# Kernel tuning notes

Hardware: AMD Instinct MI355X
Metric: run time of the kernel (lower is better)

The kernel has to match this reference:

```python
import jax, jax.numpy as jnp
import numpy as np

B, S, HID = 4, 2048, 768
NUM_HEADS = 12
HEAD_DIM = HID // NUM_HEADS


def setup_inputs() -> dict:
    key = jax.random.key(0)
    ks = jax.random.split(key, 9)
    sc = 1.0 / np.sqrt(HID)
    return {
        "x":  jax.random.normal(ks[0], (B, S, HID), dtype=jnp.float32),
        "Wq": jax.random.normal(ks[1], (HID, HID), dtype=jnp.float32) * sc,
        "bq": jnp.zeros((HID,), dtype=jnp.float32),
        "Wk": jax.random.normal(ks[2], (HID, HID), dtype=jnp.float32) * sc,
        "bk": jnp.zeros((HID,), dtype=jnp.float32),
        "Wv": jax.random.normal(ks[3], (HID, HID), dtype=jnp.float32) * sc,
        "bv": jnp.zeros((HID,), dtype=jnp.float32),
        "Wo": jax.random.normal(ks[4], (HID, HID), dtype=jnp.float32) * sc,
        "bo": jnp.zeros((HID,), dtype=jnp.float32),
    }


def _split_heads(t):
    # [B, S, HID] -> [B, H, S, D]
    b, s, _ = t.shape
    return t.reshape(b, s, NUM_HEADS, HEAD_DIM).transpose(0, 2, 1, 3)


def reference(x, Wq, bq, Wk, bk, Wv, bv, Wo, bo):
    # QKV projections (torch Linear: y = x @ W.T + b; here W stored as [in, out])
    q = _split_heads(x @ Wq + bq)
    k = _split_heads(x @ Wk + bk)
    v = _split_heads(x @ Wv + bv)
    # scaled dot-product attention scores [B, H, S, S]
    scores = jnp.einsum("bhqd,bhkd->bhqk", q, k) / jnp.sqrt(jnp.float32(HEAD_DIM))
    attn = jax.nn.softmax(scores, axis=-1)
    # dropout prob is 0.0 in the source -> identity
    ctx = jnp.einsum("bhqk,bhkd->bhqd", attn, v)
    ctx = ctx.transpose(0, 2, 1, 3).reshape(x.shape[0], x.shape[1], HID)
    out = ctx @ Wo + bo
    return out, attn
```

## Files before the change

### kernel.cpp

```cpp
#include <hip/hip_runtime.h>
#include <hip/hip_bf16.h>

typedef __bf16 bf16;
typedef __bf16 bf16x8 __attribute__((ext_vector_type(8)));
typedef float  f32x4  __attribute__((ext_vector_type(4)));

#define NB   4
#define NS   2048
#define NH   12
#define ND   64
#define NHID 768
#define NM   (NB*NS)

__device__ __forceinline__ void async_cp16(void* lds, const void* g) {
  __builtin_amdgcn_global_load_lds(
      (const __attribute__((address_space(1))) void*)g,
      (__attribute__((address_space(3))) void*)lds, 16, 0, 0);
}

__device__ __forceinline__ f32x4 mfma16(bf16x8 a, bf16x8 b, f32x4 c) {
  return __builtin_amdgcn_mfma_f32_16x16x32_bf16(a, b, c, 0, 0, 0);
}

__global__ void k_cvt_x(const float4* __restrict__ x, bf16* __restrict__ o) {
  int i = blockIdx.x * 256 + threadIdx.x;
  float4 v = x[i];
  bf16* p = o + (size_t)i * 4;
  p[0] = (bf16)v.x; p[1] = (bf16)v.y; p[2] = (bf16)v.z; p[3] = (bf16)v.w;
}

__global__ void k_trans_w(const float* __restrict__ W0, const float* __restrict__ W1,
                          const float* __restrict__ W2, const float* __restrict__ W3,
                          bf16* __restrict__ T0, bf16* __restrict__ T1,
                          bf16* __restrict__ T2, bf16* __restrict__ T3) {
  int z = blockIdx.z;
  const float* W = (z==0)?W0:(z==1)?W1:(z==2)?W2:W3;
  bf16*        T = (z==0)?T0:(z==1)?T1:(z==2)?T2:T3;
  __shared__ float t[32][33];
  int tx = threadIdx.x & 31, ty = threadIdx.x >> 5;
  int n0 = blockIdx.x * 32, k0 = blockIdx.y * 32;
  for (int i = 0; i < 32; i += 8)
    t[ty + i][tx] = W[(size_t)(k0 + ty + i) * NHID + n0 + tx];
  __syncthreads();
  for (int i = 0; i < 32; i += 8)
    T[(size_t)(n0 + ty + i) * NHID + k0 + tx] = (bf16)t[tx][ty + i];
}

__launch_bounds__(256, 2)
__global__ void k_proj(const bf16* __restrict__ xb,
                       const bf16* __restrict__ Wtq, const bf16* __restrict__ Wtk,
                       const bf16* __restrict__ Wtv,
                       const float* __restrict__ bq, const float* __restrict__ bk,
                       const float* __restrict__ bv,
                       bf16* __restrict__ qo, bf16* __restrict__ ko, bf16* __restrict__ vto) {
  const int z = blockIdx.z;
  const bf16*  Wt   = (z==0)?Wtq:(z==1)?Wtk:Wtv;
  const float* bias = (z==0)?bq :(z==1)?bk :bv;
  __shared__ __align__(16) bf16 As[128*32];
  __shared__ __align__(16) bf16 Bs[128*32];
  const int tid = threadIdx.x, w = tid >> 6, l = tid & 63;
  const int m0 = blockIdx.y * 128, n0 = blockIdx.x * 128;

  const int lr = tid >> 2, lc = tid & 3;
  const bf16* agp[2]; const bf16* bgp[2]; char* alds[2]; char* blds[2];
  for (int i = 0; i < 2; i++) {
    int r = i * 64 + lr;
    int cl = lc ^ (r & 3);
    agp[i] = xb + (size_t)(m0 + r) * NHID + cl * 8;
    bgp[i] = Wt + (size_t)(n0 + r) * NHID + cl * 8;
    alds[i] = (char*)As + i * 4096 + w * 1024;
    blds[i] = (char*)Bs + i * 4096 + w * 1024;
  }
  const int fch = ((l >> 4) ^ (l & 3)) * 8;
  const int wm = (w >> 1) * 64, wn = (w & 1) * 64;
  int aoff[4], boff[4];
  for (int i = 0; i < 4; i++) {
    aoff[i] = (wm + i * 16 + (l & 15)) * 32 + fch;
    boff[i] = (wn + i * 16 + (l & 15)) * 32 + fch;
  }
  f32x4 acc[4][4];
  f32x4 zf = {0.f, 0.f, 0.f, 0.f};
  for (int i = 0; i < 4; i++) for (int j = 0; j < 4; j++) acc[i][j] = zf;

  for (int kt = 0; kt < NHID / 32; kt++) {
    __syncthreads();
    const size_t ko2 = (size_t)kt * 32;
    for (int i = 0; i < 2; i++) {
      async_cp16(alds[i], agp[i] + ko2);
      async_cp16(blds[i], bgp[i] + ko2);
    }
    __syncthreads();
    bf16x8 af[4], bfr[4];
    for (int i = 0; i < 4; i++) af[i]  = *(const bf16x8*)(As + aoff[i]);
    for (int i = 0; i < 4; i++) bfr[i] = *(const bf16x8*)(Bs + boff[i]);
    for (int i = 0; i < 4; i++)
      for (int j = 0; j < 4; j++)
        acc[i][j] = mfma16(af[i], bfr[j], acc[i][j]);
  }
  bf16* outp = (z==0)?qo:(z==1)?ko:vto;
  for (int i = 0; i < 4; i++) {
    int mrow0 = m0 + wm + i * 16 + (l >> 4) * 4;
    for (int j = 0; j < 4; j++) {
      int col = n0 + wn + j * 16 + (l & 15);
      float bb = bias[col];
      int h = col >> 6, d = col & 63;
      for (int r = 0; r < 4; r++) {
        int m = mrow0 + r;
        int b = m >> 11, s = m & 2047;
        float v = acc[i][j][r] + bb;
        size_t idx;
        if (z < 2) idx = ((size_t)(b * NH + h) * NS + s) * ND + d;
        else       idx = ((size_t)(b * NH + h) * ND + d) * NS + s;
        outp[idx] = (bf16)v;
      }
    }
  }
}

__launch_bounds__(256, 2)
__global__ void k_rowsum(const bf16* __restrict__ qg, const bf16* __restrict__ kg,
                         float* __restrict__ rowsum) {
  const int bh = blockIdx.y;
  const int q0 = blockIdx.x * 128;
  __shared__ __align__(16) bf16 Qs[128*64];
  __shared__ __align__(16) bf16 Ks[128*64];
  const int tid = threadIdx.x, w = tid >> 6, l = tid & 63;
  const int lr8 = tid >> 3, lc8 = tid & 7;

  const bf16* qbase = qg + ((size_t)bh * NS + q0) * ND;
  for (int i = 0; i < 4; i++) {
    int r = i * 32 + lr8;
    int cl = lc8 ^ (r & 7);
    async_cp16((char*)Qs + i * 4096 + w * 1024, qbase + (size_t)r * ND + cl * 8);
  }
  int aoff[2][2], boff[8][2];
  for (int rb = 0; rb < 2; rb++)
    for (int ks = 0; ks < 2; ks++) {
      int row = w * 32 + rb * 16 + (l & 15);
      int ph = (ks * 4 + (l >> 4)) ^ (l & 7);
      aoff[rb][ks] = row * 64 + ph * 8;
    }
  for (int cb = 0; cb < 8; cb++)
    for (int ks = 0; ks < 2; ks++) {
      int row = cb * 16 + (l & 15);
      int ph = (ks * 4 + (l >> 4)) ^ (l & 7);
      boff[cb][ks] = row * 64 + ph * 8;
    }
  bf16x8 aq[2][2];
  float rs[2][4];
  for (int rb = 0; rb < 2; rb++) for (int r = 0; r < 4; r++) rs[rb][r] = 0.f;

  for (int kt = 0; kt < NS / 128; kt++) {
    __syncthreads();
    const bf16* kbase = kg + ((size_t)bh * NS + kt * 128) * ND;
    for (int i = 0; i < 4; i++) {
      int r = i * 32 + lr8;
      int cl = lc8 ^ (r & 7);
      async_cp16((char*)Ks + i * 4096 + w * 1024, kbase + (size_t)r * ND + cl * 8);
    }
    __syncthreads();
    if (kt == 0)
      for (int rb = 0; rb < 2; rb++)
        for (int ks = 0; ks < 2; ks++)
          aq[rb][ks] = *(const bf16x8*)(Qs + aoff[rb][ks]);
    for (int cb = 0; cb < 8; cb++) {
      bf16x8 b0 = *(const bf16x8*)(Ks + boff[cb][0]);
      bf16x8 b1 = *(const bf16x8*)(Ks + boff[cb][1]);
      for (int rb = 0; rb < 2; rb++) {
        f32x4 acc = {0.f, 0.f, 0.f, 0.f};
        acc = mfma16(aq[rb][0], b0, acc);
        acc = mfma16(aq[rb][1], b1, acc);
        for (int r = 0; r < 4; r++) rs[rb][r] += __expf(acc[r] * 0.125f);
      }
    }
  }
  for (int m = 1; m < 16; m <<= 1)
    for (int rb = 0; rb < 2; rb++)
      for (int r = 0; r < 4; r++)
        rs[rb][r] += __shfl_xor(rs[rb][r], m, 64);
  if ((l & 15) == 0)
    for (int rb = 0; rb < 2; rb++)
      for (int r = 0; r < 4; r++)
        rowsum[(size_t)bh * NS + q0 + w * 32 + rb * 16 + (l >> 4) * 4 + r] = rs[rb][r];
}

__launch_bounds__(256, 2)
__global__ void k_attn(const bf16* __restrict__ qg, const bf16* __restrict__ kg,
                       const bf16* __restrict__ vtg, const float* __restrict__ rowsum,
                       float* __restrict__ attn, bf16* __restrict__ ctxo) {
  const int bh = blockIdx.y;
  const int q0 = blockIdx.x * 128;
  __shared__ __align__(16) bf16 Qs[128*64];
  __shared__ __align__(16) bf16 Ks[128*64];
  __shared__ __align__(16) bf16 Vs[64*128];
  __shared__ __align__(16) bf16 Ps[4][32*40];
  __shared__ float Rs[128];
  const int tid = threadIdx.x, w = tid >> 6, l = tid & 63;

  if (tid < 128) Rs[tid] = 1.f / rowsum[(size_t)bh * NS + q0 + tid];

  const int lr8 = tid >> 3, lc8 = tid & 7;
  const int lr16 = tid >> 4, lc16 = tid & 15;
  const bf16* qbase = qg + ((size_t)bh * NS + q0) * ND;
  for (int i = 0; i < 4; i++) {
    int r = i * 32 + lr8;
    int cl = lc8 ^ (r & 7);
    async_cp16((char*)Qs + i * 4096 + w * 1024, qbase + (size_t)r * ND + cl * 8);
  }
  int aoff[2][2], boff[8][2];
  for (int rb = 0; rb < 2; rb++)
    for (int ks = 0; ks < 2; ks++) {
      int row = w * 32 + rb * 16 + (l & 15);
      int ph = (ks * 4 + (l >> 4)) ^ (l & 7);
      aoff[rb][ks] = row * 64 + ph * 8;
    }
  for (int cb = 0; cb < 8; cb++)
    for (int ks = 0; ks < 2; ks++) {
      int row = cb * 16 + (l & 15);
      int ph = (ks * 4 + (l >> 4)) ^ (l & 7);
      boff[cb][ks] = row * 64 + ph * 8;
    }
  bf16x8 aq[2][2];
  float rv[2][4];
  f32x4 ctx[2][4];
  f32x4 zf = {0.f, 0.f, 0.f, 0.f};
  for (int i = 0; i < 2; i++) for (int j = 0; j < 4; j++) ctx[i][j] = zf;

  for (int kt = 0; kt < NS / 128; kt++) {
    __syncthreads();
    const bf16* kbase = kg + ((size_t)bh * NS + kt * 128) * ND;
    for (int i = 0; i < 4; i++) {
      int r = i * 32 + lr8;
      int cl = lc8 ^ (r & 7);
      async_cp16((char*)Ks + i * 4096 + w * 1024, kbase + (size_t)r * ND + cl * 8);
    }
    const bf16* vbase = vtg + (size_t)bh * ND * NS + (size_t)kt * 128;
    for (int i = 0; i < 4; i++) {
      int r = i * 16 + lr16;
      int cl = lc16 ^ (r & 15);
      async_cp16((char*)Vs + i * 4096 + w * 1024, vbase + (size_t)r * NS + cl * 8);
    }
    __syncthreads();
    if (kt == 0) {
      for (int rb = 0; rb < 2; rb++)
        for (int ks = 0; ks < 2; ks++)
          aq[rb][ks] = *(const bf16x8*)(Qs + aoff[rb][ks]);
      for (int rb = 0; rb < 2; rb++)
        for (int r = 0; r < 4; r++)
          rv[rb][r] = Rs[w * 32 + rb * 16 + (l >> 4) * 4 + r];
    }
    const size_t arow0 = (size_t)bh * NS + q0 + w * 32;
    for (int ks2 = 0; ks2 < 4; ks2++) {
      for (int cc = 0; cc < 2; cc++) {
        int cb = ks2 * 2 + cc;
        bf16x8 b0 = *(const bf16x8*)(Ks + boff[cb][0]);
        bf16x8 b1 = *(const bf16x8*)(Ks + boff[cb][1]);
        for (int rb = 0; rb < 2; rb++) {
          f32x4 acc = {0.f, 0.f, 0.f, 0.f};
          acc = mfma16(aq[rb][0], b0, acc);
          acc = mfma16(aq[rb][1], b1, acc);
          int rloc = rb * 16 + (l >> 4) * 4;
          for (int r = 0; r < 4; r++) {
            float p = __expf(acc[r] * 0.125f) * rv[rb][r];
            attn[(arow0 + rloc + r) * NS + (size_t)kt * 128 + cb * 16 + (l & 15)] = p;
            Ps[w][(rloc + r) * 40 + cc * 16 + (l & 15)] = (bf16)p;
          }
        }
      }
      bf16x8 pa[2];
      for (int rb = 0; rb < 2; rb++)
        pa[rb] = *(const bf16x8*)(&Ps[w][(rb * 16 + (l & 15)) * 40 + (l >> 4) * 8]);
      for (int db = 0; db < 4; db++) {
        int dd = db * 16 + (l & 15);
        int ph = (ks2 * 4 + (l >> 4)) ^ (l & 15);
        bf16x8 vb = *(const bf16x8*)(Vs + dd * 128 + ph * 8);
        for (int rb = 0; rb < 2; rb++)
          ctx[rb][db] = mfma16(pa[rb], vb, ctx[rb][db]);
      }
    }
  }
  const int b = bh / NH, h = bh - b * NH;
  for (int rb = 0; rb < 2; rb++) {
    int qrow0 = q0 + w * 32 + rb * 16 + (l >> 4) * 4;
    for (int db = 0; db < 4; db++) {
      int dd = db * 16 + (l & 15);
      for (int r = 0; r < 4; r++)
        ctxo[((size_t)(b * NS + qrow0 + r)) * NHID + h * ND + dd] = (bf16)ctx[rb][db][r];
    }
  }
}

__launch_bounds__(256, 2)
__global__ void k_oproj(const bf16* __restrict__ cb_, const bf16* __restrict__ Wto,
                        const float* __restrict__ bo, float* __restrict__ out) {
  __shared__ __align__(16) bf16 As[128*32];
  __shared__ __align__(16) bf16 Bs[128*32];
  const int tid = threadIdx.x, w = tid >> 6, l = tid & 63;
  const int m0 = blockIdx.y * 128, n0 = blockIdx.x * 128;
  const int lr = tid >> 2, lc = tid & 3;
  const bf16* agp[2]; const bf16* bgp[2]; char* alds[2]; char* blds[2];
  for (int i = 0; i < 2; i++) {
    int r = i * 64 + lr;
    int cl = lc ^ (r & 3);
    agp[i] = cb_ + (size_t)(m0 + r) * NHID + cl * 8;
    bgp[i] = Wto + (size_t)(n0 + r) * NHID + cl * 8;
    alds[i] = (char*)As + i * 4096 + w * 1024;
    blds[i] = (char*)Bs + i * 4096 + w * 1024;
  }
  const int fch = ((l >> 4) ^ (l & 3)) * 8;
  const int wm = (w >> 1) * 64, wn = (w & 1) * 64;
  int aoff[4], boff[4];
  for (int i = 0; i < 4; i++) {
    aoff[i] = (wm + i * 16 + (l & 15)) * 32 + fch;
    boff[i] = (wn + i * 16 + (l & 15)) * 32 + fch;
  }
  f32x4 acc[4][4];
  f32x4 zf = {0.f, 0.f, 0.f, 0.f};
  for (int i = 0; i < 4; i++) for (int j = 0; j < 4; j++) acc[i][j] = zf;

  for (int kt = 0; kt < NHID / 32; kt++) {
    __syncthreads();
    const size_t ko2 = (size_t)kt * 32;
    for (int i = 0; i < 2; i++) {
      async_cp16(alds[i], agp[i] + ko2);
      async_cp16(blds[i], bgp[i] + ko2);
    }
    __syncthreads();
    bf16x8 af[4], bfr[4];
    for (int i = 0; i < 4; i++) af[i]  = *(const bf16x8*)(As + aoff[i]);
    for (int i = 0; i < 4; i++) bfr[i] = *(const bf16x8*)(Bs + boff[i]);
    for (int i = 0; i < 4; i++)
      for (int j = 0; j < 4; j++)
        acc[i][j] = mfma16(af[i], bfr[j], acc[i][j]);
  }
  for (int i = 0; i < 4; i++) {
    int mrow0 = m0 + wm + i * 16 + (l >> 4) * 4;
    for (int j = 0; j < 4; j++) {
      int col = n0 + wn + j * 16 + (l & 15);
      float bb = bo[col];
      for (int r = 0; r < 4; r++)
        out[(size_t)(mrow0 + r) * NHID + col] = acc[i][j][r] + bb;
    }
  }
}

extern "C" void kernel_launch(void* const* d_in, const int* in_sizes, int n_in,
                              void* d_out, int out_size, void* d_ws, size_t ws_size,
                              hipStream_t stream) {
  const float* x  = (const float*)d_in[0];
  const float* Wq = (const float*)d_in[1];
  const float* bq = (const float*)d_in[2];
  const float* Wk = (const float*)d_in[3];
  const float* bk = (const float*)d_in[4];
  const float* Wv = (const float*)d_in[5];
  const float* bv = (const float*)d_in[6];
  const float* Wo = (const float*)d_in[7];
  const float* bo = (const float*)d_in[8];
  float* out  = (float*)d_out;
  float* attn = out + (size_t)NB * NS * NHID;

  char* ws = (char*)d_ws;
  const size_t XB = (size_t)NM * NHID * 2;
  const size_t WB = (size_t)NHID * NHID * 2;
  const size_t QB = (size_t)NB * NH * NS * ND * 2;
  bf16* xb  = (bf16*)(ws);
  bf16* Wtq = (bf16*)(ws + XB);
  bf16* Wtk = (bf16*)(ws + XB + WB);
  bf16* Wtv = (bf16*)(ws + XB + 2 * WB);
  bf16* Wto = (bf16*)(ws + XB + 3 * WB);
  bf16* qw  = (bf16*)(ws + XB + 4 * WB);
  bf16* kw  = (bf16*)(ws + XB + 4 * WB + QB);
  bf16* vtw = (bf16*)(ws + XB + 4 * WB + 2 * QB);
  bf16* ctx = (bf16*)(ws + XB + 4 * WB + 3 * QB);
  float* rsum = (float*)(ws + XB + 4 * WB + 4 * QB);

  hipLaunchKernelGGL(k_cvt_x, dim3(NM * NHID / 1024), dim3(256), 0, stream,
                     (const float4*)x, xb);
  hipLaunchKernelGGL(k_trans_w, dim3(24, 24, 4), dim3(256), 0, stream,
                     Wq, Wk, Wv, Wo, Wtq, Wtk, Wtv, Wto);
  hipLaunchKernelGGL(k_proj, dim3(NHID / 128, NM / 128, 3), dim3(256), 0, stream,
                     xb, Wtq, Wtk, Wtv, bq, bk, bv, qw, kw, vtw);
  hipLaunchKernelGGL(k_rowsum, dim3(NS / 128, NB * NH), dim3(256), 0, stream,
                     qw, kw, rsum);
  hipLaunchKernelGGL(k_attn, dim3(NS / 128, NB * NH), dim3(256), 0, stream,
                     qw, kw, vtw, rsum, attn, ctx);
  hipLaunchKernelGGL(k_oproj, dim3(NHID / 128, NM / 128), dim3(256), 0, stream,
                     ctx, Wto, bo, out);
}
```

Before: 1.088 ms.

## Double-buffer LDS tiles, remap block IDs for XCD locality, prioritise MFMA waves

```diff
diff --git a/kernel.cpp b/kernel.cpp
--- a/kernel.cpp
+++ b/kernel.cpp
@@ -20,6 +20,11 @@
 
 __device__ __forceinline__ f32x4 mfma16(bf16x8 a, bf16x8 b, f32x4 c) {
   return __builtin_amdgcn_mfma_f32_16x16x32_bf16(a, b, c, 0, 0, 0);
+}
+
+__device__ __forceinline__ void vm0_bar() {
+  asm volatile("s_waitcnt vmcnt(0)" ::: "memory");
+  __builtin_amdgcn_s_barrier();
 }
 
 __global__ void k_cvt_x(const float4* __restrict__ x, bf16* __restrict__ o) {
@@ -53,24 +58,33 @@
                        const float* __restrict__ bq, const float* __restrict__ bk,
                        const float* __restrict__ bv,
                        bf16* __restrict__ qo, bf16* __restrict__ ko, bf16* __restrict__ vto) {
-  const int z = blockIdx.z;
+  const int id = blockIdx.x;
+  const int kx = id & 7, sl = id >> 3;
+  const int my = (sl / 18) * 8 + kx;
+  const int r2 = sl % 18;
+  const int nx = r2 % 6, z = r2 / 6;
   const bf16*  Wt   = (z==0)?Wtq:(z==1)?Wtk:Wtv;
   const float* bias = (z==0)?bq :(z==1)?bk :bv;
-  __shared__ __align__(16) bf16 As[128*32];
-  __shared__ __align__(16) bf16 Bs[128*32];
+  __shared__ __align__(16) bf16 As[2][128*32];
+  __shared__ __align__(16) bf16 Bs[2][128*32];
   const int tid = threadIdx.x, w = tid >> 6, l = tid & 63;
-  const int m0 = blockIdx.y * 128, n0 = blockIdx.x * 128;
+  const int m0 = my * 128, n0 = nx * 128;
 
   const int lr = tid >> 2, lc = tid & 3;
-  const bf16* agp[2]; const bf16* bgp[2]; char* alds[2]; char* blds[2];
+  const bf16* agp[2]; const bf16* bgp[2];
   for (int i = 0; i < 2; i++) {
     int r = i * 64 + lr;
     int cl = lc ^ (r & 3);
     agp[i] = xb + (size_t)(m0 + r) * NHID + cl * 8;
     bgp[i] = Wt + (size_t)(n0 + r) * NHID + cl * 8;
-    alds[i] = (char*)As + i * 4096 + w * 1024;
-    blds[i] = (char*)Bs + i * 4096 + w * 1024;
-  }
+  }
+  auto stage = [&](int b, int kt) {
+    const size_t ko2 = (size_t)kt * 32;
+    for (int i = 0; i < 2; i++) {
+      async_cp16((char*)As + b * 8192 + i * 4096 + w * 1024, agp[i] + ko2);
+      async_cp16((char*)Bs + b * 8192 + i * 4096 + w * 1024, bgp[i] + ko2);
+    }
+  };
   const int fch = ((l >> 4) ^ (l & 3)) * 8;
   const int wm = (w >> 1) * 64, wn = (w & 1) * 64;
   int aoff[4], boff[4];
@@ -82,20 +96,20 @@
   f32x4 zf = {0.f, 0.f, 0.f, 0.f};
   for (int i = 0; i < 4; i++) for (int j = 0; j < 4; j++) acc[i][j] = zf;
 
+  stage(0, 0);
+  vm0_bar();
   for (int kt = 0; kt < NHID / 32; kt++) {
-    __syncthreads();
-    const size_t ko2 = (size_t)kt * 32;
-    for (int i = 0; i < 2; i++) {
-      async_cp16(alds[i], agp[i] + ko2);
-      async_cp16(blds[i], bgp[i] + ko2);
-    }
-    __syncthreads();
+    const int cur = kt & 1;
+    if (kt < NHID / 32 - 1) stage(cur ^ 1, kt + 1);
+    const bf16* Ab = &As[cur][0];
+    const bf16* Bb = &Bs[cur][0];
     bf16x8 af[4], bfr[4];
-    for (int i = 0; i < 4; i++) af[i]  = *(const bf16x8*)(As + aoff[i]);
-    for (int i = 0; i < 4; i++) bfr[i] = *(const bf16x8*)(Bs + boff[i]);
+    for (int i = 0; i < 4; i++) af[i]  = *(const bf16x8*)(Ab + aoff[i]);
+    for (int i = 0; i < 4; i++) bfr[i] = *(const bf16x8*)(Bb + boff[i]);
     for (int i = 0; i < 4; i++)
       for (int j = 0; j < 4; j++)
         acc[i][j] = mfma16(af[i], bfr[j], acc[i][j]);
+    vm0_bar();
   }
   bf16* outp = (z==0)?qo:(z==1)?ko:vto;
   for (int i = 0; i < 4; i++) {
@@ -117,62 +131,61 @@
   }
 }
 
-__launch_bounds__(256, 2)
+__launch_bounds__(256, 4)
 __global__ void k_rowsum(const bf16* __restrict__ qg, const bf16* __restrict__ kg,
                          float* __restrict__ rowsum) {
-  const int bh = blockIdx.y;
-  const int q0 = blockIdx.x * 128;
-  __shared__ __align__(16) bf16 Qs[128*64];
-  __shared__ __align__(16) bf16 Ks[128*64];
+  const int L = blockIdx.x;
+  const int bh = ((L >> 7) << 3) | (L & 7);
+  const int q0 = ((L >> 3) & 15) * 128;
+  __shared__ __align__(16) bf16 Ks[2][128*64];
   const int tid = threadIdx.x, w = tid >> 6, l = tid & 63;
   const int lr8 = tid >> 3, lc8 = tid & 7;
 
-  const bf16* qbase = qg + ((size_t)bh * NS + q0) * ND;
-  for (int i = 0; i < 4; i++) {
-    int r = i * 32 + lr8;
-    int cl = lc8 ^ (r & 7);
-    async_cp16((char*)Qs + i * 4096 + w * 1024, qbase + (size_t)r * ND + cl * 8);
-  }
-  int aoff[2][2], boff[8][2];
+  bf16x8 aq[2][2];
   for (int rb = 0; rb < 2; rb++)
-    for (int ks = 0; ks < 2; ks++) {
-      int row = w * 32 + rb * 16 + (l & 15);
-      int ph = (ks * 4 + (l >> 4)) ^ (l & 7);
-      aoff[rb][ks] = row * 64 + ph * 8;
-    }
+    for (int ks = 0; ks < 2; ks++)
+      aq[rb][ks] = *(const bf16x8*)(qg +
+          ((size_t)bh * NS + q0 + w * 32 + rb * 16 + (l & 15)) * ND +
+          ks * 32 + (l >> 4) * 8);
+
+  int boff[8][2];
   for (int cb = 0; cb < 8; cb++)
     for (int ks = 0; ks < 2; ks++) {
       int row = cb * 16 + (l & 15);
       int ph = (ks * 4 + (l >> 4)) ^ (l & 7);
       boff[cb][ks] = row * 64 + ph * 8;
     }
-  bf16x8 aq[2][2];
-  float rs[2][4];
-  for (int rb = 0; rb < 2; rb++) for (int r = 0; r < 4; r++) rs[rb][r] = 0.f;
-
-  for (int kt = 0; kt < NS / 128; kt++) {
-    __syncthreads();
+  auto stageK = [&](int b, int kt) {
     const bf16* kbase = kg + ((size_t)bh * NS + kt * 128) * ND;
     for (int i = 0; i < 4; i++) {
       int r = i * 32 + lr8;
       int cl = lc8 ^ (r & 7);
-      async_cp16((char*)Ks + i * 4096 + w * 1024, kbase + (size_t)r * ND + cl * 8);
-    }
-    __syncthreads();
-    if (kt == 0)
-      for (int rb = 0; rb < 2; rb++)
-        for (int ks = 0; ks < 2; ks++)
-          aq[rb][ks] = *(const bf16x8*)(Qs + aoff[rb][ks]);
+      async_cp16((char*)Ks + b * 16384 + i * 4096 + w * 1024,
+                 kbase + (size_t)r * ND + cl * 8);
+    }
+  };
+  float rs[2][4];
+  for (int rb = 0; rb < 2; rb++) for (int r = 0; r < 4; r++) rs[rb][r] = 0.f;
+
+  stageK(0, 0);
+  vm0_bar();
+  for (int kt = 0; kt < NS / 128; kt++) {
+    const int cur = kt & 1;
+    if (kt < NS / 128 - 1) stageK(cur ^ 1, kt + 1);
+    const bf16* Kb = &Ks[cur][0];
     for (int cb = 0; cb < 8; cb++) {
-      bf16x8 b0 = *(const bf16x8*)(Ks + boff[cb][0]);
-      bf16x8 b1 = *(const bf16x8*)(Ks + boff[cb][1]);
+      bf16x8 b0 = *(const bf16x8*)(Kb + boff[cb][0]);
+      bf16x8 b1 = *(const bf16x8*)(Kb + boff[cb][1]);
       for (int rb = 0; rb < 2; rb++) {
         f32x4 acc = {0.f, 0.f, 0.f, 0.f};
+        __builtin_amdgcn_s_setprio(1);
         acc = mfma16(aq[rb][0], b0, acc);
         acc = mfma16(aq[rb][1], b1, acc);
+        __builtin_amdgcn_s_setprio(0);
         for (int r = 0; r < 4; r++) rs[rb][r] += __expf(acc[r] * 0.125f);
       }
     }
+    vm0_bar();
   }
   for (int m = 1; m < 16; m <<= 1)
     for (int rb = 0; rb < 2; rb++)
@@ -188,77 +201,75 @@
 __global__ void k_attn(const bf16* __restrict__ qg, const bf16* __restrict__ kg,
                        const bf16* __restrict__ vtg, const float* __restrict__ rowsum,
                        float* __restrict__ attn, bf16* __restrict__ ctxo) {
-  const int bh = blockIdx.y;
-  const int q0 = blockIdx.x * 128;
-  __shared__ __align__(16) bf16 Qs[128*64];
-  __shared__ __align__(16) bf16 Ks[128*64];
-  __shared__ __align__(16) bf16 Vs[64*128];
+  const int L = blockIdx.x;
+  const int bh = ((L >> 7) << 3) | (L & 7);
+  const int q0 = ((L >> 3) & 15) * 128;
+  __shared__ __align__(16) bf16 Ks[2][128*64];
+  __shared__ __align__(16) bf16 Vs[2][64*128];
   __shared__ __align__(16) bf16 Ps[4][32*40];
-  __shared__ float Rs[128];
   const int tid = threadIdx.x, w = tid >> 6, l = tid & 63;
-
-  if (tid < 128) Rs[tid] = 1.f / rowsum[(size_t)bh * NS + q0 + tid];
-
   const int lr8 = tid >> 3, lc8 = tid & 7;
   const int lr16 = tid >> 4, lc16 = tid & 15;
-  const bf16* qbase = qg + ((size_t)bh * NS + q0) * ND;
-  for (int i = 0; i < 4; i++) {
-    int r = i * 32 + lr8;
-    int cl = lc8 ^ (r & 7);
-    async_cp16((char*)Qs + i * 4096 + w * 1024, qbase + (size_t)r * ND + cl * 8);
-  }
-  int aoff[2][2], boff[8][2];
-  for (int rb = 0; rb < 2; rb++)
-    for (int ks = 0; ks < 2; ks++) {
-      int row = w * 32 + rb * 16 + (l & 15);
-      int ph = (ks * 4 + (l >> 4)) ^ (l & 7);
-      aoff[rb][ks] = row * 64 + ph * 8;
-    }
+
+  bf16x8 aq[2][2];
+  float rv[2][4];
+  for (int rb = 0; rb < 2; rb++) {
+    for (int ks = 0; ks < 2; ks++)
+      aq[rb][ks] = *(const bf16x8*)(qg +
+          ((size_t)bh * NS + q0 + w * 32 + rb * 16 + (l & 15)) * ND +
+          ks * 32 + (l >> 4) * 8);
+    for (int r = 0; r < 4; r++)
+      rv[rb][r] = 1.f / rowsum[(size_t)bh * NS + q0 + w * 32 + rb * 16 + (l >> 4) * 4 + r];
+  }
+
+  int boff[8][2];
   for (int cb = 0; cb < 8; cb++)
     for (int ks = 0; ks < 2; ks++) {
       int row = cb * 16 + (l & 15);
       int ph = (ks * 4 + (l >> 4)) ^ (l & 7);
       boff[cb][ks] = row * 64 + ph * 8;
     }
-  bf16x8 aq[2][2];
-  float rv[2][4];
-  f32x4 ctx[2][4];
-  f32x4 zf = {0.f, 0.f, 0.f, 0.f};
-  for (int i = 0; i < 2; i++) for (int j = 0; j < 4; j++) ctx[i][j] = zf;
-
-  for (int kt = 0; kt < NS / 128; kt++) {
-    __syncthreads();
+  auto stageK = [&](int b, int kt) {
     const bf16* kbase = kg + ((size_t)bh * NS + kt * 128) * ND;
     for (int i = 0; i < 4; i++) {
       int r = i * 32 + lr8;
       int cl = lc8 ^ (r & 7);
-      async_cp16((char*)Ks + i * 4096 + w * 1024, kbase + (size_t)r * ND + cl * 8);
-    }
+      async_cp16((char*)Ks + b * 16384 + i * 4096 + w * 1024,
+                 kbase + (size_t)r * ND + cl * 8);
+    }
+  };
+  auto stageV = [&](int b, int kt) {
     const bf16* vbase = vtg + (size_t)bh * ND * NS + (size_t)kt * 128;
     for (int i = 0; i < 4; i++) {
       int r = i * 16 + lr16;
       int cl = lc16 ^ (r & 15);
-      async_cp16((char*)Vs + i * 4096 + w * 1024, vbase + (size_t)r * NS + cl * 8);
-    }
-    __syncthreads();
-    if (kt == 0) {
-      for (int rb = 0; rb < 2; rb++)
-        for (int ks = 0; ks < 2; ks++)
-          aq[rb][ks] = *(const bf16x8*)(Qs + aoff[rb][ks]);
-      for (int rb = 0; rb < 2; rb++)
-        for (int r = 0; r < 4; r++)
-          rv[rb][r] = Rs[w * 32 + rb * 16 + (l >> 4) * 4 + r];
-    }
-    const size_t arow0 = (size_t)bh * NS + q0 + w * 32;
+      async_cp16((char*)Vs + b * 16384 + i * 4096 + w * 1024,
+                 vbase + (size_t)r * NS + cl * 8);
+    }
+  };
+  f32x4 ctx[2][4];
+  f32x4 zf = {0.f, 0.f, 0.f, 0.f};
+  for (int i = 0; i < 2; i++) for (int j = 0; j < 4; j++) ctx[i][j] = zf;
+
+  stageK(0, 0); stageV(0, 0);
+  vm0_bar();
+  const size_t arow0 = (size_t)bh * NS + q0 + w * 32;
+  for (int kt = 0; kt < NS / 128; kt++) {
+    const int cur = kt & 1;
+    if (kt < NS / 128 - 1) { stageK(cur ^ 1, kt + 1); stageV(cur ^ 1, kt + 1); }
+    const bf16* Kb = &Ks[cur][0];
+    const bf16* Vb = &Vs[cur][0];
     for (int ks2 = 0; ks2 < 4; ks2++) {
       for (int cc = 0; cc < 2; cc++) {
         int cb = ks2 * 2 + cc;
-        bf16x8 b0 = *(const bf16x8*)(Ks + boff[cb][0]);
-        bf16x8 b1 = *(const bf16x8*)(Ks + boff[cb][1]);
+        bf16x8 b0 = *(const bf16x8*)(Kb + boff[cb][0]);
+        bf16x8 b1 = *(const bf16x8*)(Kb + boff[cb][1]);
         for (int rb = 0; rb < 2; rb++) {
           f32x4 acc = {0.f, 0.f, 0.f, 0.f};
+          __builtin_amdgcn_s_setprio(1);
           acc = mfma16(aq[rb][0], b0, acc);
           acc = mfma16(aq[rb][1], b1, acc);
+          __builtin_amdgcn_s_setprio(0);
           int rloc = rb * 16 + (l >> 4) * 4;
           for (int r = 0; r < 4; r++) {
             float p = __expf(acc[r] * 0.125f) * rv[rb][r];
@@ -270,14 +281,17 @@
       bf16x8 pa[2];
       for (int rb = 0; rb < 2; rb++)
         pa[rb] = *(const bf16x8*)(&Ps[w][(rb * 16 + (l & 15)) * 40 + (l >> 4) * 8]);
+      __builtin_amdgcn_s_setprio(1);
       for (int db = 0; db < 4; db++) {
         int dd = db * 16 + (l & 15);
         int ph = (ks2 * 4 + (l >> 4)) ^ (l & 15);
-        bf16x8 vb = *(const bf16x8*)(Vs + dd * 128 + ph * 8);
+        bf16x8 vb = *(const bf16x8*)(Vb + dd * 128 + ph * 8);
         for (int rb = 0; rb < 2; rb++)
           ctx[rb][db] = mfma16(pa[rb], vb, ctx[rb][db]);
       }
-    }
+      __builtin_amdgcn_s_setprio(0);
+    }
+    vm0_bar();
   }
   const int b = bh / NH, h = bh - b * NH;
   for (int rb = 0; rb < 2; rb++) {
@@ -293,20 +307,29 @@
 __launch_bounds__(256, 2)
 __global__ void k_oproj(const bf16* __restrict__ cb_, const bf16* __restrict__ Wto,
                         const float* __restrict__ bo, float* __restrict__ out) {
-  __shared__ __align__(16) bf16 As[128*32];
-  __shared__ __align__(16) bf16 Bs[128*32];
+  const int id = blockIdx.x;
+  const int kx = id & 7, sl = id >> 3;
+  const int my = (sl / 6) * 8 + kx;
+  const int nx = sl % 6;
+  __shared__ __align__(16) bf16 As[2][128*32];
+  __shared__ __align__(16) bf16 Bs[2][128*32];
   const int tid = threadIdx.x, w = tid >> 6, l = tid & 63;
-  const int m0 = blockIdx.y * 128, n0 = blockIdx.x * 128;
+  const int m0 = my * 128, n0 = nx * 128;
   const int lr = tid >> 2, lc = tid & 3;
-  const bf16* agp[2]; const bf16* bgp[2]; char* alds[2]; char* blds[2];
+  const bf16* agp[2]; const bf16* bgp[2];
   for (int i = 0; i < 2; i++) {
     int r = i * 64 + lr;
     int cl = lc ^ (r & 3);
     agp[i] = cb_ + (size_t)(m0 + r) * NHID + cl * 8;
     bgp[i] = Wto + (size_t)(n0 + r) * NHID + cl * 8;
-    alds[i] = (char*)As + i * 4096 + w * 1024;
-    blds[i] = (char*)Bs + i * 4096 + w * 1024;
-  }
+  }
+  auto stage = [&](int b, int kt) {
+    const size_t ko2 = (size_t)kt * 32;
+    for (int i = 0; i < 2; i++) {
+      async_cp16((char*)As + b * 8192 + i * 4096 + w * 1024, agp[i] + ko2);
+      async_cp16((char*)Bs + b * 8192 + i * 4096 + w * 1024, bgp[i] + ko2);
+    }
+  };
   const int fch = ((l >> 4) ^ (l & 3)) * 8;
   const int wm = (w >> 1) * 64, wn = (w & 1) * 64;
   int aoff[4], boff[4];
@@ -318,20 +341,20 @@
   f32x4 zf = {0.f, 0.f, 0.f, 0.f};
   for (int i = 0; i < 4; i++) for (int j = 0; j < 4; j++) acc[i][j] = zf;
 
+  stage(0, 0);
+  vm0_bar();
   for (int kt = 0; kt < NHID / 32; kt++) {
-    __syncthreads();
-    const size_t ko2 = (size_t)kt * 32;
-    for (int i = 0; i < 2; i++) {
-      async_cp16(alds[i], agp[i] + ko2);
-      async_cp16(blds[i], bgp[i] + ko2);
-    }
-    __syncthreads();
+    const int cur = kt & 1;
+    if (kt < NHID / 32 - 1) stage(cur ^ 1, kt + 1);
+    const bf16* Ab = &As[cur][0];
+    const bf16* Bb = &Bs[cur][0];
     bf16x8 af[4], bfr[4];
-    for (int i = 0; i < 4; i++) af[i]  = *(const bf16x8*)(As + aoff[i]);
-    for (int i = 0; i < 4; i++) bfr[i] = *(const bf16x8*)(Bs + boff[i]);
+    for (int i = 0; i < 4; i++) af[i]  = *(const bf16x8*)(Ab + aoff[i]);
+    for (int i = 0; i < 4; i++) bfr[i] = *(const bf16x8*)(Bb + boff[i]);
     for (int i = 0; i < 4; i++)
       for (int j = 0; j < 4; j++)
         acc[i][j] = mfma16(af[i], bfr[j], acc[i][j]);
+    vm0_bar();
   }
   for (int i = 0; i < 4; i++) {
     int mrow0 = m0 + wm + i * 16 + (l >> 4) * 4;
@@ -378,12 +401,12 @@
                      (const float4*)x, xb);
   hipLaunchKernelGGL(k_trans_w, dim3(24, 24, 4), dim3(256), 0, stream,
                      Wq, Wk, Wv, Wo, Wtq, Wtk, Wtv, Wto);
-  hipLaunchKernelGGL(k_proj, dim3(NHID / 128, NM / 128, 3), dim3(256), 0, stream,
+  hipLaunchKernelGGL(k_proj, dim3(1152), dim3(256), 0, stream,
                      xb, Wtq, Wtk, Wtv, bq, bk, bv, qw, kw, vtw);
-  hipLaunchKernelGGL(k_rowsum, dim3(NS / 128, NB * NH), dim3(256), 0, stream,
+  hipLaunchKernelGGL(k_rowsum, dim3(768), dim3(256), 0, stream,
                      qw, kw, rsum);
-  hipLaunchKernelGGL(k_attn, dim3(NS / 128, NB * NH), dim3(256), 0, stream,
+  hipLaunchKernelGGL(k_attn, dim3(768), dim3(256), 0, stream,
                      qw, kw, vtw, rsum, attn, ctx);
-  hipLaunchKernelGGL(k_oproj, dim3(NHID / 128, NM / 128), dim3(256), 0, stream,
+  hipLaunchKernelGGL(k_oproj, dim3(384), dim3(256), 0, stream,
                      ctx, Wto, bo, out);
 }
```

Result: no change. 1.071 ms (-1.5%).
